# Optimization experiments

Measured on AMD Instinct MI355X. Metric: run time of the kernel, lower is better.

Reference implementation:

```python
import jax, jax.numpy as jnp
import numpy as np

D_MODEL = 256
D_STATE = 16
D_CONV = 3
D_INNER = 256          # expand=1
D_HALF = D_INNER // 2  # 128
DT_RANK = 16           # ceil(256/16)
B, L0, L1 = 4, 4096, 4096


def setup_inputs() -> dict:
    key = jax.random.key(0)
    ks = jax.random.split(key, 10)
    u_0 = jax.random.normal(ks[0], (B, L0, D_MODEL), jnp.float32)
    u_1 = jax.random.normal(ks[1], (B, L1, D_MODEL), jnp.float32)
    in_proj_w = jax.random.normal(ks[2], (D_INNER, D_MODEL), jnp.float32) * (D_MODEL ** -0.5)
    conv_x_w = jax.random.normal(ks[3], (D_HALF, 1, D_CONV), jnp.float32) * (D_CONV ** -0.5)
    conv_z_w = jax.random.normal(ks[4], (D_HALF, 1, D_CONV), jnp.float32) * (D_CONV ** -0.5)
    x_proj_w = jax.random.normal(ks[5], (DT_RANK + 2 * D_STATE, D_HALF), jnp.float32) * (D_HALF ** -0.5)
    dt_init_std = DT_RANK ** -0.5
    dt_proj_w = jax.random.uniform(ks[6], (D_HALF, DT_RANK), jnp.float32, -dt_init_std, dt_init_std)
    # dt bias = inverse-softplus of dt ~ LogUniform(1e-3, 1e-1)
    dt = jnp.exp(jax.random.uniform(ks[7], (D_HALF,), jnp.float32) * (np.log(0.1) - np.log(0.001)) + np.log(0.001))
    dt = jnp.clip(dt, 1e-4, None)
    dt_proj_b = dt + jnp.log(-jnp.expm1(-dt))
    A_log = jnp.log(jnp.broadcast_to(jnp.arange(1, D_STATE + 1, dtype=jnp.float32), (D_HALF, D_STATE)))
    D_param = jnp.ones((D_HALF,), jnp.float32)
    out_proj_w = jax.random.normal(ks[8], (D_MODEL, D_INNER), jnp.float32) * (D_INNER ** -0.5)
    return {"u_0": u_0, "u_1": u_1, "in_proj_w": in_proj_w, "conv_x_w": conv_x_w,
            "conv_z_w": conv_z_w, "x_proj_w": x_proj_w, "dt_proj_w": dt_proj_w,
            "dt_proj_b": dt_proj_b, "A_log": A_log, "D": D_param, "out_proj_w": out_proj_w}


def _dwconv(x, w):
    # x: [B, C, L], w: [C, 1, K] depthwise, padding='same', no bias (conv_bias//2 == 0)
    return jax.lax.conv_general_dilated(
        x, w, window_strides=(1,), padding='SAME',
        feature_group_count=x.shape[1], dimension_numbers=('NCH', 'OIH', 'NCH'))


def _selective_scan(u, delta, A, Bm, Cm, Dv):
    # u, delta: [B, L, d]; A: [d, n]; Bm, Cm: [B, L, n]; Dv: [d]
    dA = jnp.exp(delta[..., None] * A)                       # [B, L, d, n]
    dBu = (delta * u)[..., None] * Bm[:, :, None, :]         # [B, L, d, n]
    def combine(c1, c2):
        a1, b1 = c1
        a2, b2 = c2
        return a2 * a1, a2 * b1 + b2
    _, h = jax.lax.associative_scan(combine, (dA, dBu), axis=1)  # h: [B, L, d, n]
    return jnp.einsum('bldn,bln->bld', h, Cm) + u * Dv


def _stream(u, in_proj_w, conv_x_w, conv_z_w, x_proj_w, dt_proj_w, dt_proj_b, A, D, out_proj_w):
    xz = jnp.einsum('bld,ed->ble', u, in_proj_w)             # [B, L, d_inner]
    x, z = jnp.split(xz, 2, axis=-1)                         # [B, L, d_half] each
    x = jnp.swapaxes(x, 1, 2)                                # [B, d_half, L]
    z = jnp.swapaxes(z, 1, 2)
    x_f = jax.nn.silu(_dwconv(x, conv_x_w))
    z_f = jax.nn.silu(_dwconv(z, conv_z_w))
    xf = jnp.swapaxes(x_f, 1, 2)                             # [B, L, d_half]
    dbl = jnp.einsum('bld,ed->ble', xf, x_proj_w)            # [B, L, dt_rank + 2n]
    dt, Bm, Cm = jnp.split(dbl, [DT_RANK, DT_RANK + D_STATE], axis=-1)
    dt = jnp.einsum('blr,dr->bld', dt, dt_proj_w)
    delta = jax.nn.softplus(dt + dt_proj_b)                  # delta_bias + delta_softplus
    y = _selective_scan(xf, delta, A, Bm, Cm, D)             # [B, L, d_half]
    cat = jnp.concatenate([y, jnp.swapaxes(z_f, 1, 2)], axis=-1)  # [B, L, d_inner]
    return jnp.einsum('ble,oe->blo', cat, out_proj_w)


def reference(u_0, u_1, in_proj_w, conv_x_w, conv_z_w, x_proj_w, dt_proj_w, dt_proj_b, A_log, D, out_proj_w):
    A = -jnp.exp(A_log)
    out0 = _stream(u_0, in_proj_w, conv_x_w, conv_z_w, x_proj_w, dt_proj_w, dt_proj_b, A, D, out_proj_w)
    out1 = _stream(u_1, in_proj_w, conv_x_w, conv_z_w, x_proj_w, dt_proj_w, dt_proj_b, A, D, out_proj_w)
    return (out0, out1)
```

## Files before the change

kernel.cpp:

```cpp
#include <hip/hip_runtime.h>
#include <hip/hip_bf16.h>
#include <cstdint>

#define DEV __device__ __forceinline__

typedef __attribute__((ext_vector_type(8))) short short8;
typedef __attribute__((ext_vector_type(4))) float f32x4;
typedef __attribute__((ext_vector_type(4))) unsigned short us4;
typedef __attribute__((ext_vector_type(8))) unsigned short us8;

DEV unsigned short f2bf(float x) {
    unsigned int u = __float_as_uint(x);
    unsigned int r = (u + 0x7FFFu + ((u >> 16) & 1u)) >> 16;
    return (unsigned short)r;
}
DEV float bf2f(unsigned short h) { return __uint_as_float(((unsigned int)h) << 16); }

#define LL 4096
#define DM 256
#define DH 128
#define NS 16
#define SB_TOT 8
#define CH1 32
#define NCH 128
#define LOG2E 1.44269504088896f

__global__ __launch_bounds__(256) void prep_kernel(
    const float* __restrict__ u0, const float* __restrict__ u1,
    const float* __restrict__ inw, const float* __restrict__ outw,
    const float* __restrict__ alog,
    const float* __restrict__ xpw, const float* __restrict__ dtw,
    unsigned short* __restrict__ ubf, unsigned short* __restrict__ wbi,
    unsigned short* __restrict__ wbo, float* __restrict__ An,
    unsigned short* __restrict__ Wb)
{
    int gid = blockIdx.x * 256 + threadIdx.x;
    int i = gid * 4;
    if (i < 4194304) {
        f32x4 v = *(const f32x4*)&u0[i];
        us4 r = { f2bf(v.x), f2bf(v.y), f2bf(v.z), f2bf(v.w) };
        *(us4*)&ubf[i] = r;
    } else if (i < 8388608) {
        int j = i - 4194304;
        f32x4 v = *(const f32x4*)&u1[j];
        us4 r = { f2bf(v.x), f2bf(v.y), f2bf(v.z), f2bf(v.w) };
        *(us4*)&ubf[4194304 + j] = r;
    } else if (i < 8454144) {
        int j = i - 8388608;
        f32x4 v = *(const f32x4*)&inw[j];
        us4 r = { f2bf(v.x), f2bf(v.y), f2bf(v.z), f2bf(v.w) };
        *(us4*)&wbi[j] = r;
    } else if (i < 8519680) {
        int j = i - 8454144;
        f32x4 v = *(const f32x4*)&outw[j];
        us4 r = { f2bf(v.x), f2bf(v.y), f2bf(v.z), f2bf(v.w) };
        *(us4*)&wbo[j] = r;
    } else if (i < 8521728) {
        int j = i - 8519680;
        f32x4 v = *(const f32x4*)&alog[j];
        f32x4 r = { -__expf(v.x), -__expf(v.y), -__expf(v.z), -__expf(v.w) };
        *(f32x4*)&An[j] = r;
    } else if (i < 8542208) {
        int j = i - 8521728;
        int n = j >> 7, k0 = j & 127;
        if (n < 128) {
            float a0 = 0.f, a1 = 0.f, a2 = 0.f, a3 = 0.f;
            const float* dw = dtw + n * 16;
            #pragma unroll
            for (int r = 0; r < 16; ++r) {
                float w = dw[r];
                const float* xr = xpw + r * 128 + k0;
                a0 = fmaf(w, xr[0], a0);
                a1 = fmaf(w, xr[1], a1);
                a2 = fmaf(w, xr[2], a2);
                a3 = fmaf(w, xr[3], a3);
            }
            us4 rr = { f2bf(a0), f2bf(a1), f2bf(a2), f2bf(a3) };
            *(us4*)&Wb[n * 128 + k0] = rr;
        } else {
            f32x4 v = *(const f32x4*)&xpw[(n - 112) * 128 + k0];
            us4 rr = { f2bf(v.x), f2bf(v.y), f2bf(v.z), f2bf(v.w) };
            *(us4*)&Wb[n * 128 + k0] = rr;
        }
    }
}

template<int F32OUT>
__global__ __launch_bounds__(256) void gemm_bt(
    const unsigned short* __restrict__ A, const unsigned short* __restrict__ B,
    float* __restrict__ Cf, unsigned short* __restrict__ Cb)
{
    __shared__ __align__(16) unsigned short As[128 * 32];
    __shared__ __align__(16) unsigned short Bs[128 * 32];
    const int t = threadIdx.x;
    const int m0 = blockIdx.x * 128, n0 = blockIdx.y * 128;
    const int lane = t & 63, wv = t >> 6;
    const int wm = (wv & 1) * 64, wn = (wv >> 1) * 64;
    const int lr = lane & 15, lk = (lane >> 4) * 8;

    f32x4 acc[4][4] = {};
    for (int kt = 0; kt < 8; ++kt) {
        const int k0 = kt * 32;
        #pragma unroll
        for (int j = 0; j < 2; ++j) {
            int c = t + j * 256;
            int row = c >> 2, col = (c & 3) * 8;
            short8 va = *(const short8*)(A + (size_t)(m0 + row) * 256 + k0 + col);
            short8 vb = *(const short8*)(B + (size_t)(n0 + row) * 256 + k0 + col);
            *(short8*)&As[row * 32 + col] = va;
            *(short8*)&Bs[row * 32 + col] = vb;
        }
        __syncthreads();
        short8 av[4], bv[4];
        #pragma unroll
        for (int i = 0; i < 4; ++i) av[i] = *(const short8*)&As[(wm + i * 16 + lr) * 32 + lk];
        #pragma unroll
        for (int i = 0; i < 4; ++i) bv[i] = *(const short8*)&Bs[(wn + i * 16 + lr) * 32 + lk];
        #pragma unroll
        for (int i = 0; i < 4; ++i)
            #pragma unroll
            for (int j = 0; j < 4; ++j)
                acc[i][j] = __builtin_amdgcn_mfma_f32_16x16x32_bf16(av[i], bv[j], acc[i][j], 0, 0, 0);
        __syncthreads();
    }
    #pragma unroll
    for (int i = 0; i < 4; ++i) {
        #pragma unroll
        for (int j = 0; j < 4; ++j) {
            int r0 = m0 + wm + i * 16 + (lane >> 4) * 4;
            int cc = n0 + wn + j * 16 + lr;
            #pragma unroll
            for (int r = 0; r < 4; ++r) {
                float v = acc[i][j][r];
                if (F32OUT) Cf[(size_t)(r0 + r) * 256 + cc] = v;
                else        Cb[(size_t)(r0 + r) * 256 + cc] = f2bf(v);
            }
        }
    }
}

__global__ __launch_bounds__(256) void conv_silu(
    const unsigned short* __restrict__ xz, const float* __restrict__ wx,
    const float* __restrict__ wz, float* __restrict__ xf, unsigned short* __restrict__ catb)
{
    int gid = blockIdx.x * 256 + threadIdx.x;
    int g = gid & 15;
    int l = (gid >> 4) & 4095;
    int sb = gid >> 16;
    size_t row = (size_t)sb * LL + l;
    const unsigned short* bp = xz + row * DM;
    int cx = g * 8;
    us8 zz = (us8)0;
    us8 xm = (l > 0)    ? *(const us8*)(bp - DM + cx)        : zz;
    us8 x0 = *(const us8*)(bp + cx);
    us8 xp = (l < 4095) ? *(const us8*)(bp + DM + cx)        : zz;
    us8 zm = (l > 0)    ? *(const us8*)(bp - DM + 128 + cx)  : zz;
    us8 z0 = *(const us8*)(bp + 128 + cx);
    us8 zp = (l < 4095) ? *(const us8*)(bp + DM + 128 + cx)  : zz;

    float xo[8]; us8 zo;
    #pragma unroll
    for (int j = 0; j < 8; ++j) {
        int c = cx + j;
        float xv = bf2f(xm[j]) * wx[c * 3] + bf2f(x0[j]) * wx[c * 3 + 1] + bf2f(xp[j]) * wx[c * 3 + 2];
        float zv = bf2f(zm[j]) * wz[c * 3] + bf2f(z0[j]) * wz[c * 3 + 1] + bf2f(zp[j]) * wz[c * 3 + 2];
        xv = xv / (1.f + __expf(-xv));
        zv = zv / (1.f + __expf(-zv));
        xo[j] = xv;
        zo[j] = f2bf(zv);
    }
    *(f32x4*)&xf[row * DH + cx]     = *(f32x4*)&xo[0];
    *(f32x4*)&xf[row * DH + cx + 4] = *(f32x4*)&xo[4];
    *(us8*)&catb[row * DM + 128 + cx] = zo;
}

__global__ __launch_bounds__(256) void proj_mfma(
    const float* __restrict__ xf, const unsigned short* __restrict__ Wb,
    const float* __restrict__ dtb,
    float* __restrict__ delta, float* __restrict__ BC)
{
    __shared__ __align__(16) unsigned short Bs[160 * 136];
    __shared__ __align__(16) unsigned short As[64 * 48];
    const int t = threadIdx.x;
    const size_t m0 = (size_t)blockIdx.x * 64;
    for (int q = t; q < 2560; q += 256) {
        int n = q >> 4, kc = (q & 15) * 8;
        *(short8*)&Bs[n * 136 + kc] = *(const short8*)(Wb + n * 128 + kc);
    }
    const int lane = t & 63, wv = t >> 6;
    const int lr = lane & 15, lk = (lane >> 4) * 8;
    const int arow = t >> 2, akc = (t & 3) * 8;
    f32x4 acc[10] = {};
    for (int kt = 0; kt < 4; ++kt) {
        const int k0 = kt * 32;
        {
            const float* src = xf + (m0 + arow) * 128 + k0 + akc;
            f32x4 v0 = *(const f32x4*)src;
            f32x4 v1 = *(const f32x4*)(src + 4);
            us8 r = { f2bf(v0.x), f2bf(v0.y), f2bf(v0.z), f2bf(v0.w),
                      f2bf(v1.x), f2bf(v1.y), f2bf(v1.z), f2bf(v1.w) };
            *(us8*)&As[arow * 48 + akc] = r;
        }
        __syncthreads();
        short8 av = *(const short8*)&As[(wv * 16 + lr) * 48 + lk];
        #pragma unroll
        for (int j = 0; j < 10; ++j) {
            short8 bv = *(const short8*)&Bs[(j * 16 + lr) * 136 + k0 + lk];
            acc[j] = __builtin_amdgcn_mfma_f32_16x16x32_bf16(av, bv, acc[j], 0, 0, 0);
        }
        __syncthreads();
    }
    const int r0 = (lane >> 4) * 4;
    #pragma unroll
    for (int j = 0; j < 10; ++j) {
        int col = j * 16 + lr;
        #pragma unroll
        for (int r = 0; r < 4; ++r) {
            float v = acc[j][r];
            size_t row = m0 + wv * 16 + r0 + r;
            if (j < 8) {
                float x = v + dtb[col];
                float sp = (x > 20.f) ? x : log1pf(__expf(x));
                delta[row * 128 + col] = sp;
            } else {
                BC[row * 32 + (col - 128)] = v;
            }
        }
    }
}

__global__ __launch_bounds__(128) void scan_p1(
    const float* __restrict__ delta, const float* __restrict__ xf,
    const float* __restrict__ BC, const float* __restrict__ An,
    float* __restrict__ P, float* __restrict__ H)
{
    __shared__ float dt_s[CH1 * 128];
    __shared__ float du_s[CH1 * 128];
    __shared__ float b_s[CH1 * 16];
    int t = threadIdx.x;
    int ch = blockIdx.x, sb = blockIdx.y;
    size_t rb = (size_t)sb * LL + (size_t)ch * CH1;
    for (int q = t; q < CH1 * 32; q += 128) {
        int row = q >> 5, c4 = (q & 31) * 4;
        f32x4 dv = *(const f32x4*)&delta[(rb + row) * DH + c4];
        f32x4 uv = *(const f32x4*)&xf[(rb + row) * DH + c4];
        *(f32x4*)&dt_s[row * 128 + c4] = dv;
        f32x4 duv = dv * uv;
        *(f32x4*)&du_s[row * 128 + c4] = duv;
    }
    {
        int q = t & 127;
        int row = q >> 2, c4 = (q & 3) * 4;
        *(f32x4*)&b_s[row * 16 + c4] = *(const f32x4*)&BC[(rb + row) * 32 + c4];
    }
    __syncthreads();
    float Ar[16];
    #pragma unroll
    for (int n = 0; n < 16; ++n) Ar[n] = An[t * 16 + n] * LOG2E;
    float h[16], p[16];
    #pragma unroll
    for (int n = 0; n < 16; ++n) { h[n] = 0.f; p[n] = 1.f; }
    for (int i = 0; i < CH1; ++i) {
        float dt = dt_s[i * 128 + t];
        float du = du_s[i * 128 + t];
        float bl[16];
        *(f32x4*)&bl[0]  = *(const f32x4*)&b_s[i * 16];
        *(f32x4*)&bl[4]  = *(const f32x4*)&b_s[i * 16 + 4];
        *(f32x4*)&bl[8]  = *(const f32x4*)&b_s[i * 16 + 8];
        *(f32x4*)&bl[12] = *(const f32x4*)&b_s[i * 16 + 12];
        #pragma unroll
        for (int n = 0; n < 16; ++n) {
            float a = exp2f(dt * Ar[n]);
            h[n] = fmaf(a, h[n], du * bl[n]);
            p[n] *= a;
        }
    }
    size_t ob = (((size_t)sb * NCH + ch) * 128 + t) * 16;
    #pragma unroll
    for (int n4 = 0; n4 < 16; n4 += 4) {
        f32x4 pv = { p[n4], p[n4 + 1], p[n4 + 2], p[n4 + 3] };
        f32x4 hv = { h[n4], h[n4 + 1], h[n4 + 2], h[n4 + 3] };
        *(f32x4*)&P[ob + n4] = pv;
        *(f32x4*)&H[ob + n4] = hv;
    }
}

__global__ __launch_bounds__(256) void scan_p2(const float* __restrict__ P, float* __restrict__ H)
{
    __shared__ float Ps[NCH * 16], Hs[NCH * 16];
    int t = threadIdx.x;
    int d = blockIdx.x, sb = blockIdx.y;
    for (int q = t; q < NCH * 4; q += 256) {
        int ch = q >> 2, c4 = (q & 3) * 4;
        size_t g = (((size_t)sb * NCH + ch) * 128 + d) * 16 + c4;
        *(f32x4*)&Ps[ch * 16 + c4] = *(const f32x4*)&P[g];
        *(f32x4*)&Hs[ch * 16 + c4] = *(const f32x4*)&H[g];
    }
    __syncthreads();
    if (t < 16) {
        float hin = 0.f;
        for (int c = 0; c < NCH; ++c) {
            float pp = Ps[c * 16 + t], hl = Hs[c * 16 + t];
            Hs[c * 16 + t] = hin;
            hin = fmaf(pp, hin, hl);
        }
    }
    __syncthreads();
    for (int q = t; q < NCH * 4; q += 256) {
        int ch = q >> 2, c4 = (q & 3) * 4;
        size_t g = (((size_t)sb * NCH + ch) * 128 + d) * 16 + c4;
        *(f32x4*)&H[g] = *(const f32x4*)&Hs[ch * 16 + c4];
    }
}

__global__ __launch_bounds__(128) void scan_p3(
    const float* __restrict__ delta, const float* __restrict__ xf,
    const float* __restrict__ BC, const float* __restrict__ An,
    const float* __restrict__ Dp, const float* __restrict__ H,
    unsigned short* __restrict__ catb)
{
    __shared__ float dt_s[CH1 * 128];
    __shared__ float u_s[CH1 * 128];
    __shared__ float b_s[CH1 * 16];
    __shared__ float c_s[CH1 * 16];
    int t = threadIdx.x;
    int ch = blockIdx.x, sb = blockIdx.y;
    size_t rb = (size_t)sb * LL + (size_t)ch * CH1;
    for (int q = t; q < CH1 * 32; q += 128) {
        int row = q >> 5, c4 = (q & 31) * 4;
        *(f32x4*)&dt_s[row * 128 + c4] = *(const f32x4*)&delta[(rb + row) * DH + c4];
        *(f32x4*)&u_s[row * 128 + c4]  = *(const f32x4*)&xf[(rb + row) * DH + c4];
    }
    {
        int q = t & 127;
        int row = q >> 2, c4 = (q & 3) * 4;
        *(f32x4*)&b_s[row * 16 + c4] = *(const f32x4*)&BC[(rb + row) * 32 + c4];
        *(f32x4*)&c_s[row * 16 + c4] = *(const f32x4*)&BC[(rb + row) * 32 + 16 + c4];
    }
    __syncthreads();
    float Ar[16];
    #pragma unroll
    for (int n = 0; n < 16; ++n) Ar[n] = An[t * 16 + n] * LOG2E;
    float Dv = Dp[t];
    size_t ob = (((size_t)sb * NCH + ch) * 128 + t) * 16;
    float h[16];
    #pragma unroll
    for (int n4 = 0; n4 < 16; n4 += 4) {
        f32x4 hv = *(const f32x4*)&H[ob + n4];
        h[n4] = hv.x; h[n4 + 1] = hv.y; h[n4 + 2] = hv.z; h[n4 + 3] = hv.w;
    }
    for (int i = 0; i < CH1; ++i) {
        float dt = dt_s[i * 128 + t];
        float uu = u_s[i * 128 + t];
        float du = dt * uu;
        float bl[16], cl[16];
        *(f32x4*)&bl[0]  = *(const f32x4*)&b_s[i * 16];
        *(f32x4*)&bl[4]  = *(const f32x4*)&b_s[i * 16 + 4];
        *(f32x4*)&bl[8]  = *(const f32x4*)&b_s[i * 16 + 8];
        *(f32x4*)&bl[12] = *(const f32x4*)&b_s[i * 16 + 12];
        *(f32x4*)&cl[0]  = *(const f32x4*)&c_s[i * 16];
        *(f32x4*)&cl[4]  = *(const f32x4*)&c_s[i * 16 + 4];
        *(f32x4*)&cl[8]  = *(const f32x4*)&c_s[i * 16 + 8];
        *(f32x4*)&cl[12] = *(const f32x4*)&c_s[i * 16 + 12];
        float y0 = uu * Dv, y1 = 0.f, y2 = 0.f, y3 = 0.f;
        #pragma unroll
        for (int n = 0; n < 16; n += 4) {
            float a0 = exp2f(dt * Ar[n]);
            float a1 = exp2f(dt * Ar[n + 1]);
            float a2 = exp2f(dt * Ar[n + 2]);
            float a3 = exp2f(dt * Ar[n + 3]);
            h[n]     = fmaf(a0, h[n],     du * bl[n]);
            h[n + 1] = fmaf(a1, h[n + 1], du * bl[n + 1]);
            h[n + 2] = fmaf(a2, h[n + 2], du * bl[n + 2]);
            h[n + 3] = fmaf(a3, h[n + 3], du * bl[n + 3]);
            y0 = fmaf(h[n],     cl[n],     y0);
            y1 = fmaf(h[n + 1], cl[n + 1], y1);
            y2 = fmaf(h[n + 2], cl[n + 2], y2);
            y3 = fmaf(h[n + 3], cl[n + 3], y3);
        }
        float y = (y0 + y1) + (y2 + y3);
        catb[(rb + i) * DM + t] = f2bf(y);
    }
}

extern "C" void kernel_launch(void* const* d_in, const int* in_sizes, int n_in,
                              void* d_out, int out_size, void* d_ws, size_t ws_size,
                              hipStream_t stream) {
    const float* u0   = (const float*)d_in[0];
    const float* u1   = (const float*)d_in[1];
    const float* inw  = (const float*)d_in[2];
    const float* cxw  = (const float*)d_in[3];
    const float* czw  = (const float*)d_in[4];
    const float* xpw  = (const float*)d_in[5];
    const float* dtw  = (const float*)d_in[6];
    const float* dtb  = (const float*)d_in[7];
    const float* alog = (const float*)d_in[8];
    const float* Dp   = (const float*)d_in[9];
    const float* outw = (const float*)d_in[10];

    char* ws = (char*)d_ws;
    unsigned short* ubf  = (unsigned short*)(ws + 0);
    float* P             = (float*)(ws + 0);
    float* H             = (float*)(ws + 8388608);
    unsigned short* xzbf = (unsigned short*)(ws + 16777216);
    float* delta         = (float*)(ws + 16777216);
    unsigned short* wbi  = (unsigned short*)(ws + 33554432);
    unsigned short* wbo  = (unsigned short*)(ws + 33685504);
    float* An            = (float*)(ws + 33816576);
    float* xf            = (float*)(ws + 33824768);
    float* BC            = (float*)(ws + 50601984);
    unsigned short* catb = (unsigned short*)(ws + 54796288);
    unsigned short* Wb   = (unsigned short*)(ws + 71573504);

    float* outp = (float*)d_out;

    prep_kernel<<<8342, 256, 0, stream>>>(u0, u1, inw, outw, alog, xpw, dtw, ubf, wbi, wbo, An, Wb);
    gemm_bt<0><<<dim3(256, 2), 256, 0, stream>>>(ubf, wbi, nullptr, xzbf);
    conv_silu<<<2048, 256, 0, stream>>>(xzbf, cxw, czw, xf, catb);
    proj_mfma<<<512, 256, 0, stream>>>(xf, Wb, dtb, delta, BC);
    scan_p1<<<dim3(NCH, 8), 128, 0, stream>>>(delta, xf, BC, An, P, H);
    scan_p2<<<dim3(128, 8), 256, 0, stream>>>(P, H);
    scan_p3<<<dim3(NCH, 8), 128, 0, stream>>>(delta, xf, BC, An, Dp, H, catb);
    gemm_bt<1><<<dim3(256, 2), 256, 0, stream>>>(catb, wbo, outp, nullptr);
}
```

Before: 231.1 us.

## Fuse input bf16 conversion into GEMMs and conv into x_proj kernel

Removes the standalone prep pass that converted u0/u1 and the weights to bf16: the GEMM now loads fp32 activations and weights directly and converts them while staging into padded shared memory. Each GEMM block also covers the full 256-column N range. The depthwise conv+SiLU is fused into the projection kernel so x is staged into LDS once rather than written out and reread. A is computed inline in the scan kernels. This cuts launches and global traffic, in exchange for redundant weight conversion per block, larger LDS use and more accumulator registers per thread.

```diff
diff --git a/kernel.cpp b/kernel.cpp
--- a/kernel.cpp
+++ b/kernel.cpp
@@ -25,110 +25,99 @@
 #define NCH 128
 #define LOG2E 1.44269504088896f
 
-__global__ __launch_bounds__(256) void prep_kernel(
-    const float* __restrict__ u0, const float* __restrict__ u1,
-    const float* __restrict__ inw, const float* __restrict__ outw,
-    const float* __restrict__ alog,
+__global__ __launch_bounds__(256) void prep_w(
     const float* __restrict__ xpw, const float* __restrict__ dtw,
-    unsigned short* __restrict__ ubf, unsigned short* __restrict__ wbi,
-    unsigned short* __restrict__ wbo, float* __restrict__ An,
     unsigned short* __restrict__ Wb)
 {
     int gid = blockIdx.x * 256 + threadIdx.x;
-    int i = gid * 4;
-    if (i < 4194304) {
-        f32x4 v = *(const f32x4*)&u0[i];
-        us4 r = { f2bf(v.x), f2bf(v.y), f2bf(v.z), f2bf(v.w) };
-        *(us4*)&ubf[i] = r;
-    } else if (i < 8388608) {
-        int j = i - 4194304;
-        f32x4 v = *(const f32x4*)&u1[j];
-        us4 r = { f2bf(v.x), f2bf(v.y), f2bf(v.z), f2bf(v.w) };
-        *(us4*)&ubf[4194304 + j] = r;
-    } else if (i < 8454144) {
-        int j = i - 8388608;
-        f32x4 v = *(const f32x4*)&inw[j];
-        us4 r = { f2bf(v.x), f2bf(v.y), f2bf(v.z), f2bf(v.w) };
-        *(us4*)&wbi[j] = r;
-    } else if (i < 8519680) {
-        int j = i - 8454144;
-        f32x4 v = *(const f32x4*)&outw[j];
-        us4 r = { f2bf(v.x), f2bf(v.y), f2bf(v.z), f2bf(v.w) };
-        *(us4*)&wbo[j] = r;
-    } else if (i < 8521728) {
-        int j = i - 8519680;
-        f32x4 v = *(const f32x4*)&alog[j];
-        f32x4 r = { -__expf(v.x), -__expf(v.y), -__expf(v.z), -__expf(v.w) };
-        *(f32x4*)&An[j] = r;
-    } else if (i < 8542208) {
-        int j = i - 8521728;
-        int n = j >> 7, k0 = j & 127;
-        if (n < 128) {
-            float a0 = 0.f, a1 = 0.f, a2 = 0.f, a3 = 0.f;
-            const float* dw = dtw + n * 16;
-            #pragma unroll
-            for (int r = 0; r < 16; ++r) {
-                float w = dw[r];
-                const float* xr = xpw + r * 128 + k0;
-                a0 = fmaf(w, xr[0], a0);
-                a1 = fmaf(w, xr[1], a1);
-                a2 = fmaf(w, xr[2], a2);
-                a3 = fmaf(w, xr[3], a3);
-            }
-            us4 rr = { f2bf(a0), f2bf(a1), f2bf(a2), f2bf(a3) };
-            *(us4*)&Wb[n * 128 + k0] = rr;
-        } else {
-            f32x4 v = *(const f32x4*)&xpw[(n - 112) * 128 + k0];
-            us4 rr = { f2bf(v.x), f2bf(v.y), f2bf(v.z), f2bf(v.w) };
-            *(us4*)&Wb[n * 128 + k0] = rr;
-        }
-    }
-}
-
-template<int F32OUT>
-__global__ __launch_bounds__(256) void gemm_bt(
-    const unsigned short* __restrict__ A, const unsigned short* __restrict__ B,
+    if (gid >= 5120) return;
+    int n = gid >> 5, k0 = (gid & 31) * 4;
+    if (n < 128) {
+        float a0 = 0.f, a1 = 0.f, a2 = 0.f, a3 = 0.f;
+        const float* dw = dtw + n * 16;
+        #pragma unroll
+        for (int r = 0; r < 16; ++r) {
+            float w = dw[r];
+            const float* xr = xpw + r * 128 + k0;
+            a0 = fmaf(w, xr[0], a0);
+            a1 = fmaf(w, xr[1], a1);
+            a2 = fmaf(w, xr[2], a2);
+            a3 = fmaf(w, xr[3], a3);
+        }
+        us4 rr = { f2bf(a0), f2bf(a1), f2bf(a2), f2bf(a3) };
+        *(us4*)&Wb[n * 128 + k0] = rr;
+    } else {
+        f32x4 v = *(const f32x4*)&xpw[(n - 112) * 128 + k0];
+        us4 rr = { f2bf(v.x), f2bf(v.y), f2bf(v.z), f2bf(v.w) };
+        *(us4*)&Wb[n * 128 + k0] = rr;
+    }
+}
+
+template<int AF32, int F32OUT>
+__global__ __launch_bounds__(256) void gemm_full(
+    const float* __restrict__ Af0, const float* __restrict__ Af1,
+    const unsigned short* __restrict__ Ab,
+    const float* __restrict__ Bw,
     float* __restrict__ Cf, unsigned short* __restrict__ Cb)
 {
-    __shared__ __align__(16) unsigned short As[128 * 32];
-    __shared__ __align__(16) unsigned short Bs[128 * 32];
+    __shared__ __align__(16) unsigned short As[128 * 40];
+    __shared__ __align__(16) unsigned short Bs[256 * 40];
     const int t = threadIdx.x;
-    const int m0 = blockIdx.x * 128, n0 = blockIdx.y * 128;
+    const int m0 = blockIdx.x * 128;
     const int lane = t & 63, wv = t >> 6;
-    const int wm = (wv & 1) * 64, wn = (wv >> 1) * 64;
+    const int wm = (wv & 1) * 64, wn = (wv >> 1) * 128;
     const int lr = lane & 15, lk = (lane >> 4) * 8;
-
-    f32x4 acc[4][4] = {};
+    const float* Afp = nullptr;
+    if (AF32) Afp = (blockIdx.x < 128) ? (Af0 + (size_t)m0 * 256)
+                                       : (Af1 + ((size_t)m0 - 16384) * 256);
+    f32x4 acc[4][8] = {};
     for (int kt = 0; kt < 8; ++kt) {
         const int k0 = kt * 32;
         #pragma unroll
-        for (int j = 0; j < 2; ++j) {
-            int c = t + j * 256;
-            int row = c >> 2, col = (c & 3) * 8;
-            short8 va = *(const short8*)(A + (size_t)(m0 + row) * 256 + k0 + col);
-            short8 vb = *(const short8*)(B + (size_t)(n0 + row) * 256 + k0 + col);
-            *(short8*)&As[row * 32 + col] = va;
-            *(short8*)&Bs[row * 32 + col] = vb;
+        for (int i = 0; i < 6; ++i) {
+            int s = t + i * 256;
+            int row = s >> 2, col = (s & 3) * 8;
+            if (row < 128) {
+                if (AF32) {
+                    const float* src = Afp + (size_t)row * 256 + k0 + col;
+                    f32x4 v0 = *(const f32x4*)src;
+                    f32x4 v1 = *(const f32x4*)(src + 4);
+                    us8 r = { f2bf(v0.x), f2bf(v0.y), f2bf(v0.z), f2bf(v0.w),
+                              f2bf(v1.x), f2bf(v1.y), f2bf(v1.z), f2bf(v1.w) };
+                    *(us8*)&As[row * 40 + col] = r;
+                } else {
+                    *(short8*)&As[row * 40 + col] =
+                        *(const short8*)(Ab + (size_t)(m0 + row) * 256 + k0 + col);
+                }
+            } else {
+                int br = row - 128;
+                const float* src = Bw + (size_t)br * 256 + k0 + col;
+                f32x4 v0 = *(const f32x4*)src;
+                f32x4 v1 = *(const f32x4*)(src + 4);
+                us8 r = { f2bf(v0.x), f2bf(v0.y), f2bf(v0.z), f2bf(v0.w),
+                          f2bf(v1.x), f2bf(v1.y), f2bf(v1.z), f2bf(v1.w) };
+                *(us8*)&Bs[br * 40 + col] = r;
+            }
         }
         __syncthreads();
-        short8 av[4], bv[4];
-        #pragma unroll
-        for (int i = 0; i < 4; ++i) av[i] = *(const short8*)&As[(wm + i * 16 + lr) * 32 + lk];
-        #pragma unroll
-        for (int i = 0; i < 4; ++i) bv[i] = *(const short8*)&Bs[(wn + i * 16 + lr) * 32 + lk];
-        #pragma unroll
-        for (int i = 0; i < 4; ++i)
+        short8 av[4];
+        #pragma unroll
+        for (int i = 0; i < 4; ++i) av[i] = *(const short8*)&As[(wm + i * 16 + lr) * 40 + lk];
+        #pragma unroll
+        for (int j = 0; j < 8; ++j) {
+            short8 bv = *(const short8*)&Bs[(wn + j * 16 + lr) * 40 + lk];
             #pragma unroll
-            for (int j = 0; j < 4; ++j)
-                acc[i][j] = __builtin_amdgcn_mfma_f32_16x16x32_bf16(av[i], bv[j], acc[i][j], 0, 0, 0);
+            for (int i = 0; i < 4; ++i)
+                acc[i][j] = __builtin_amdgcn_mfma_f32_16x16x32_bf16(av[i], bv, acc[i][j], 0, 0, 0);
+        }
         __syncthreads();
     }
     #pragma unroll
     for (int i = 0; i < 4; ++i) {
         #pragma unroll
-        for (int j = 0; j < 4; ++j) {
+        for (int j = 0; j < 8; ++j) {
             int r0 = m0 + wm + i * 16 + (lane >> 4) * 4;
-            int cc = n0 + wn + j * 16 + lr;
+            int cc = wn + j * 16 + lr;
             #pragma unroll
             for (int r = 0; r < 4; ++r) {
                 float v = acc[i][j][r];
@@ -139,76 +128,66 @@
     }
 }
 
-__global__ __launch_bounds__(256) void conv_silu(
-    const unsigned short* __restrict__ xz, const float* __restrict__ wx,
-    const float* __restrict__ wz, float* __restrict__ xf, unsigned short* __restrict__ catb)
-{
-    int gid = blockIdx.x * 256 + threadIdx.x;
-    int g = gid & 15;
-    int l = (gid >> 4) & 4095;
-    int sb = gid >> 16;
-    size_t row = (size_t)sb * LL + l;
-    const unsigned short* bp = xz + row * DM;
-    int cx = g * 8;
-    us8 zz = (us8)0;
-    us8 xm = (l > 0)    ? *(const us8*)(bp - DM + cx)        : zz;
-    us8 x0 = *(const us8*)(bp + cx);
-    us8 xp = (l < 4095) ? *(const us8*)(bp + DM + cx)        : zz;
-    us8 zm = (l > 0)    ? *(const us8*)(bp - DM + 128 + cx)  : zz;
-    us8 z0 = *(const us8*)(bp + 128 + cx);
-    us8 zp = (l < 4095) ? *(const us8*)(bp + DM + 128 + cx)  : zz;
-
-    float xo[8]; us8 zo;
-    #pragma unroll
-    for (int j = 0; j < 8; ++j) {
-        int c = cx + j;
-        float xv = bf2f(xm[j]) * wx[c * 3] + bf2f(x0[j]) * wx[c * 3 + 1] + bf2f(xp[j]) * wx[c * 3 + 2];
-        float zv = bf2f(zm[j]) * wz[c * 3] + bf2f(z0[j]) * wz[c * 3 + 1] + bf2f(zp[j]) * wz[c * 3 + 2];
-        xv = xv / (1.f + __expf(-xv));
-        zv = zv / (1.f + __expf(-zv));
-        xo[j] = xv;
-        zo[j] = f2bf(zv);
-    }
-    *(f32x4*)&xf[row * DH + cx]     = *(f32x4*)&xo[0];
-    *(f32x4*)&xf[row * DH + cx + 4] = *(f32x4*)&xo[4];
-    *(us8*)&catb[row * DM + 128 + cx] = zo;
-}
-
-__global__ __launch_bounds__(256) void proj_mfma(
-    const float* __restrict__ xf, const unsigned short* __restrict__ Wb,
+__global__ __launch_bounds__(256) void convproj(
+    const unsigned short* __restrict__ xz, const unsigned short* __restrict__ Wb,
+    const float* __restrict__ wx, const float* __restrict__ wz,
     const float* __restrict__ dtb,
+    float* __restrict__ xf, unsigned short* __restrict__ catb,
     float* __restrict__ delta, float* __restrict__ BC)
 {
     __shared__ __align__(16) unsigned short Bs[160 * 136];
-    __shared__ __align__(16) unsigned short As[64 * 48];
+    __shared__ __align__(16) unsigned short As[64 * 136];
     const int t = threadIdx.x;
-    const size_t m0 = (size_t)blockIdx.x * 64;
+    const int m0 = blockIdx.x * 64;
     for (int q = t; q < 2560; q += 256) {
         int n = q >> 4, kc = (q & 15) * 8;
         *(short8*)&Bs[n * 136 + kc] = *(const short8*)(Wb + n * 128 + kc);
     }
+    #pragma unroll
+    for (int i = 0; i < 8; ++i) {
+        int s = t + i * 256;
+        int r = s >> 5, g = s & 31;
+        int gr = m0 + r;
+        int l = gr & 4095;
+        int c; const float* wp; const unsigned short* bp;
+        if (g < 16) { c = g * 8;        wp = wx; bp = xz + (size_t)gr * 256 + c; }
+        else        { c = (g - 16) * 8; wp = wz; bp = xz + (size_t)gr * 256 + 128 + c; }
+        us8 zz = (us8)0;
+        us8 vm = (l > 0)    ? *(const us8*)(bp - 256) : zz;
+        us8 v0 = *(const us8*)bp;
+        us8 vp = (l < 4095) ? *(const us8*)(bp + 256) : zz;
+        float o[8];
+        #pragma unroll
+        for (int j = 0; j < 8; ++j) {
+            int cc = c + j;
+            float v = bf2f(vm[j]) * wp[cc * 3] + bf2f(v0[j]) * wp[cc * 3 + 1]
+                    + bf2f(vp[j]) * wp[cc * 3 + 2];
+            v = v / (1.f + __expf(-v));
+            o[j] = v;
+        }
+        us8 rb = { f2bf(o[0]), f2bf(o[1]), f2bf(o[2]), f2bf(o[3]),
+                   f2bf(o[4]), f2bf(o[5]), f2bf(o[6]), f2bf(o[7]) };
+        if (g < 16) {
+            *(us8*)&As[r * 136 + c] = rb;
+            *(f32x4*)&xf[(size_t)gr * 128 + c]     = *(f32x4*)&o[0];
+            *(f32x4*)&xf[(size_t)gr * 128 + c + 4] = *(f32x4*)&o[4];
+        } else {
+            *(us8*)&catb[(size_t)gr * 256 + 128 + c] = rb;
+        }
+    }
+    __syncthreads();
     const int lane = t & 63, wv = t >> 6;
     const int lr = lane & 15, lk = (lane >> 4) * 8;
-    const int arow = t >> 2, akc = (t & 3) * 8;
     f32x4 acc[10] = {};
+    #pragma unroll
     for (int kt = 0; kt < 4; ++kt) {
         const int k0 = kt * 32;
-        {
-            const float* src = xf + (m0 + arow) * 128 + k0 + akc;
-            f32x4 v0 = *(const f32x4*)src;
-            f32x4 v1 = *(const f32x4*)(src + 4);
-            us8 r = { f2bf(v0.x), f2bf(v0.y), f2bf(v0.z), f2bf(v0.w),
-                      f2bf(v1.x), f2bf(v1.y), f2bf(v1.z), f2bf(v1.w) };
-            *(us8*)&As[arow * 48 + akc] = r;
-        }
-        __syncthreads();
-        short8 av = *(const short8*)&As[(wv * 16 + lr) * 48 + lk];
+        short8 av = *(const short8*)&As[(wv * 16 + lr) * 136 + k0 + lk];
         #pragma unroll
         for (int j = 0; j < 10; ++j) {
             short8 bv = *(const short8*)&Bs[(j * 16 + lr) * 136 + k0 + lk];
             acc[j] = __builtin_amdgcn_mfma_f32_16x16x32_bf16(av, bv, acc[j], 0, 0, 0);
         }
-        __syncthreads();
     }
     const int r0 = (lane >> 4) * 4;
     #pragma unroll
@@ -217,7 +196,7 @@
         #pragma unroll
         for (int r = 0; r < 4; ++r) {
             float v = acc[j][r];
-            size_t row = m0 + wv * 16 + r0 + r;
+            size_t row = (size_t)m0 + wv * 16 + r0 + r;
             if (j < 8) {
                 float x = v + dtb[col];
                 float sp = (x > 20.f) ? x : log1pf(__expf(x));
@@ -231,7 +210,7 @@
 
 __global__ __launch_bounds__(128) void scan_p1(
     const float* __restrict__ delta, const float* __restrict__ xf,
-    const float* __restrict__ BC, const float* __restrict__ An,
+    const float* __restrict__ BC, const float* __restrict__ alog,
     float* __restrict__ P, float* __restrict__ H)
 {
     __shared__ float dt_s[CH1 * 128];
@@ -256,7 +235,7 @@
     __syncthreads();
     float Ar[16];
     #pragma unroll
-    for (int n = 0; n < 16; ++n) Ar[n] = An[t * 16 + n] * LOG2E;
+    for (int n = 0; n < 16; ++n) Ar[n] = -__expf(alog[t * 16 + n]) * LOG2E;
     float h[16], p[16];
     #pragma unroll
     for (int n = 0; n < 16; ++n) { h[n] = 0.f; p[n] = 1.f; }
@@ -315,7 +294,7 @@
 
 __global__ __launch_bounds__(128) void scan_p3(
     const float* __restrict__ delta, const float* __restrict__ xf,
-    const float* __restrict__ BC, const float* __restrict__ An,
+    const float* __restrict__ BC, const float* __restrict__ alog,
     const float* __restrict__ Dp, const float* __restrict__ H,
     unsigned short* __restrict__ catb)
 {
@@ -340,7 +319,7 @@
     __syncthreads();
     float Ar[16];
     #pragma unroll
-    for (int n = 0; n < 16; ++n) Ar[n] = An[t * 16 + n] * LOG2E;
+    for (int n = 0; n < 16; ++n) Ar[n] = -__expf(alog[t * 16 + n]) * LOG2E;
     float Dv = Dp[t];
     size_t ob = (((size_t)sb * NCH + ch) * 128 + t) * 16;
     float h[16];
@@ -399,27 +378,22 @@
     const float* outw = (const float*)d_in[10];
 
     char* ws = (char*)d_ws;
-    unsigned short* ubf  = (unsigned short*)(ws + 0);
+    unsigned short* xzbf = (unsigned short*)(ws + 0);
     float* P             = (float*)(ws + 0);
     float* H             = (float*)(ws + 8388608);
-    unsigned short* xzbf = (unsigned short*)(ws + 16777216);
     float* delta         = (float*)(ws + 16777216);
-    unsigned short* wbi  = (unsigned short*)(ws + 33554432);
-    unsigned short* wbo  = (unsigned short*)(ws + 33685504);
-    float* An            = (float*)(ws + 33816576);
-    float* xf            = (float*)(ws + 33824768);
-    float* BC            = (float*)(ws + 50601984);
-    unsigned short* catb = (unsigned short*)(ws + 54796288);
-    unsigned short* Wb   = (unsigned short*)(ws + 71573504);
+    float* xf            = (float*)(ws + 33554432);
+    float* BC            = (float*)(ws + 50331648);
+    unsigned short* catb = (unsigned short*)(ws + 54525952);
+    unsigned short* Wb   = (unsigned short*)(ws + 71303168);
 
     float* outp = (float*)d_out;
 
-    prep_kernel<<<8342, 256, 0, stream>>>(u0, u1, inw, outw, alog, xpw, dtw, ubf, wbi, wbo, An, Wb);
-    gemm_bt<0><<<dim3(256, 2), 256, 0, stream>>>(ubf, wbi, nullptr, xzbf);
-    conv_silu<<<2048, 256, 0, stream>>>(xzbf, cxw, czw, xf, catb);
-    proj_mfma<<<512, 256, 0, stream>>>(xf, Wb, dtb, delta, BC);
-    scan_p1<<<dim3(NCH, 8), 128, 0, stream>>>(delta, xf, BC, An, P, H);
+    prep_w<<<20, 256, 0, stream>>>(xpw, dtw, Wb);
+    gemm_full<1, 0><<<256, 256, 0, stream>>>(u0, u1, nullptr, inw, nullptr, xzbf);
+    convproj<<<512, 256, 0, stream>>>(xzbf, Wb, cxw, czw, dtb, xf, catb, delta, BC);
+    scan_p1<<<dim3(NCH, 8), 128, 0, stream>>>(delta, xf, BC, alog, P, H);
     scan_p2<<<dim3(128, 8), 256, 0, stream>>>(P, H);
-    scan_p3<<<dim3(NCH, 8), 128, 0, stream>>>(delta, xf, BC, An, Dp, H, catb);
-    gemm_bt<1><<<dim3(256, 2), 256, 0, stream>>>(catb, wbo, outp, nullptr);
-}
+    scan_p3<<<dim3(NCH, 8), 128, 0, stream>>>(delta, xf, BC, alog, Dp, H, catb);
+    gemm_full<0, 1><<<256, 256, 0, stream>>>(nullptr, nullptr, catb, outw, outp, nullptr);
+}
```

After: 237.1 us. 2.6% more time.
